# Kernel tuning notes

Measured on AMD Instinct MI355X. Metric: run time of the kernel, lower is better.

The kernel has to match this reference:

```python
import jax, jax.numpy as jnp
import numpy as np

N_NODES = 100000   # number of graph nodes
N_EDGES = 1000000  # number of edges
D_IN = 64          # input feature dim
D_OUT = 64         # output feature dim
N_RELS = 16        # number of relation types


def setup_inputs() -> dict:
    key = jax.random.key(0)
    k1, k2, k3, k4, k5 = jax.random.split(key, 5)
    feat = jax.random.normal(k1, (N_NODES, D_IN), dtype=jnp.float32)
    weight = jax.random.normal(k2, (N_RELS, D_IN, D_OUT), dtype=jnp.float32) * 0.05
    src = jax.random.randint(k3, (N_EDGES,), 0, N_NODES)
    dst = jax.random.randint(k4, (N_EDGES,), 0, N_NODES)
    etypes = jax.random.randint(k5, (N_EDGES,), 0, N_RELS)
    return {"feat": feat, "weight": weight, "src": src, "dst": dst, "etypes": etypes}


def reference(feat, weight, src, dst, etypes):
    # gather source-node features per edge: h = edges.src['h']
    h = feat[src]                                # [E, d_in]
    n_rels = weight.shape[0]
    e, d_out = h.shape[0], weight.shape[2]

    # gather_mm(h, weight, idx_b=etypes): m_e = h_e @ weight[etypes_e]
    # grouped-GEMM realized as R masked dense GEMMs (R is small, fixed);
    # avoids materializing the [E, d_in, d_out] gathered weight tensor.
    def step(m, rw):
        r, w_r = rw
        mask = jnp.where(etypes == r, 1.0, 0.0).astype(h.dtype)  # [E]
        m = m + mask[:, None] * (h @ w_r)                        # [E, d_out]
        return m, None

    m0 = jnp.zeros((e, d_out), dtype=h.dtype)
    m, _ = jax.lax.scan(step, m0, (jnp.arange(n_rels), weight))

    # update_all(..., fn.sum('m', 'h')): scatter-sum messages to dst nodes
    out = jax.ops.segment_sum(m, dst, num_segments=feat.shape[0])  # [N, d_out]
    return out
```

## Files before the change

kernel.cpp:

```cpp
#include <hip/hip_runtime.h>
#include <hip/hip_bf16.h>
#include <stdint.h>

#define NNODES 100000
#define NEDGES 1000000
#define NRELS 16
#define EPB 2048
#define NB ((NEDGES + EPB - 1) / EPB)
#define PADCAP (NEDGES + NRELS * 64)
#define MAXTILES (PADCAP / 64)
#define NDN NNODES
#define BKT 256
#define NBKT ((NDN + BKT - 1) / BKT)

#define FEAT_BLKS 6250
#define W_BLKS 256
#define SETUP_BLKS (FEAT_BLKS + W_BLKS + NB)
#define SCANS_BLKS (1 + (NBKT + 15) / 16)

#define WS_NEED 157070848ull

using short8  = __attribute__((ext_vector_type(8))) short;
using floatx4 = __attribute__((ext_vector_type(4))) float;
using uintx4  = __attribute__((ext_vector_type(4))) unsigned int;

__device__ __forceinline__ unsigned short f2bf(float f) {
    union { float f; uint32_t u; } v; v.f = f;
    uint32_t u = v.u;
    return (unsigned short)((u + 0x7FFFu + ((u >> 16) & 1u)) >> 16);
}
__device__ __forceinline__ float bf2f(uint32_t u16) {
    union { uint32_t u; float f; } v; v.u = u16 << 16;
    return v.f;
}
__device__ __forceinline__ uint32_t pk2(float a, float b) {
    __hip_bfloat162 h = __float22bfloat162_rn(make_float2(a, b));
    union { __hip_bfloat162 h; uint32_t u; } v; v.h = h;
    return v.u;
}

__global__ void k_setup(const float* __restrict__ feat, const float* __restrict__ W,
                        const int* __restrict__ et, const int* __restrict__ dst,
                        unsigned short* __restrict__ featB, unsigned short* __restrict__ Wt,
                        int* __restrict__ hist16, int* __restrict__ hist391) {
    __shared__ int cnt16[16];
    __shared__ int cnt391[NBKT];
    const int b = blockIdx.x;
    if (b < FEAT_BLKS) {
        int i = (b * 256 + threadIdx.x) * 4;
        const float4 f = *(const float4*)(feat + i);
        ushort4 o;
        o.x = f2bf(f.x); o.y = f2bf(f.y); o.z = f2bf(f.z); o.w = f2bf(f.w);
        *(ushort4*)(featB + i) = o;
    } else if (b < FEAT_BLKS + W_BLKS) {
        int t = (b - FEAT_BLKS) * 256 + threadIdx.x;
        int r = t >> 12, n = (t >> 6) & 63, k = t & 63;
        Wt[t] = f2bf(W[(r << 12) + (k << 6) + n]);
    } else {
        const int bb = b - (FEAT_BLKS + W_BLKS);
        if (threadIdx.x < 16) cnt16[threadIdx.x] = 0;
        for (int t = threadIdx.x; t < NBKT; t += 256) cnt391[t] = 0;
        __syncthreads();
        int start = bb * EPB;
        int end = min(NEDGES, start + EPB);
        for (int i = start + threadIdx.x; i < end; i += 256) {
            atomicAdd(&cnt16[et[i]], 1);
            atomicAdd(&cnt391[dst[i] >> 8], 1);
        }
        __syncthreads();
        if (threadIdx.x < 16) hist16[bb * 16 + threadIdx.x] = cnt16[threadIdx.x];
        for (int t = threadIdx.x; t < NBKT; t += 256)
            hist391[bb * NBKT + t] = cnt391[t];
    }
}

__global__ void __launch_bounds__(1024)
k_scans(const int* __restrict__ hist16, int* __restrict__ bbase16,
        int* __restrict__ Pve,
        const int* __restrict__ hist391, int* __restrict__ bbase391,
        int* __restrict__ bstart) {
    int w = threadIdx.x >> 6;
    int lane = threadIdx.x & 63;
    if (blockIdx.x == 0) {
        __shared__ int s_cnt[16];
        __shared__ int s_P[17];
        int carry = 0;
        for (int c = 0; c < NB; c += 64) {
            int idx = c + lane;
            int v = (idx < NB) ? hist16[idx * 16 + w] : 0;
            int x = v;
            #pragma unroll
            for (int off = 1; off < 64; off <<= 1) {
                int y = __shfl_up(x, off);
                if (lane >= off) x += y;
            }
            if (idx < NB) bbase16[idx * 16 + w] = carry + x - v;
            carry += __shfl(x, 63);
        }
        if (lane == 0) s_cnt[w] = carry;
        __syncthreads();
        if (threadIdx.x == 0) {
            int p = 0;
            for (int r = 0; r < 16; ++r) {
                s_P[r] = p;
                Pve[r] = p;
                Pve[17 + r] = p + s_cnt[r];
                p += (s_cnt[r] + 63) & ~63;
            }
            s_P[16] = p;
            Pve[16] = p;
        }
        __syncthreads();
        int pw = s_P[w];
        for (int idx = lane; idx < NB; idx += 64)
            bbase16[idx * 16 + w] += pw;
    } else {
        int b = (blockIdx.x - 1) * 16 + w;
        if (b >= NBKT) return;
        int carry = 0;
        for (int c = 0; c < NB; c += 64) {
            int idx = c + lane;
            int v = (idx < NB) ? hist391[idx * NBKT + b] : 0;
            int x = v;
            #pragma unroll
            for (int off = 1; off < 64; off <<= 1) {
                int y = __shfl_up(x, off);
                if (lane >= off) x += y;
            }
            if (idx < NB) bbase391[idx * NBKT + b] = carry + x - v;
            carry += __shfl(x, 63);
        }
        if (lane == 0) bstart[b] = carry;
    }
}

__global__ void k_bscanB(int* __restrict__ bstart) {
    __shared__ int wtot[8];
    int t = threadIdx.x;
    int v = (t < NBKT) ? bstart[t] : 0;
    int lane = t & 63, w = t >> 6;
    int x = v;
    #pragma unroll
    for (int off = 1; off < 64; off <<= 1) {
        int y = __shfl_up(x, off);
        if (lane >= off) x += y;
    }
    if (lane == 63) wtot[w] = x;
    __syncthreads();
    int woff = 0;
    for (int i = 0; i < w; ++i) woff += wtot[i];
    if (t < NBKT) bstart[t] = woff + x - v;
    if (t == 511) {
        int total = 0;
        for (int i = 0; i < 8; ++i) total += wtot[i];
        bstart[NBKT] = total;
    }
}

__global__ void k_scatter(const int* __restrict__ et, const int* __restrict__ src,
                          const int* __restrict__ dst, const int* __restrict__ bbase16,
                          const int* __restrict__ bbase391, const int* __restrict__ bstart,
                          int* __restrict__ srcS, int* __restrict__ keyE,
                          unsigned short* __restrict__ dnode) {
    __shared__ int base16[16];
    __shared__ int base391[NBKT];
    if (threadIdx.x < 16) base16[threadIdx.x] = bbase16[blockIdx.x * 16 + threadIdx.x];
    for (int t = threadIdx.x; t < NBKT; t += 256)
        base391[t] = bbase391[blockIdx.x * NBKT + t] + bstart[t];
    __syncthreads();
    int start = blockIdx.x * EPB;
    int end = min(NEDGES, start + EPB);
    for (int i = start + threadIdx.x; i < end; i += 256) {
        int r = et[i];
        int pos = atomicAdd(&base16[r], 1);
        srcS[pos] = src[i];
        int d = dst[i];
        int bp = atomicAdd(&base391[d >> 8], 1);
        keyE[bp] = pos;
        dnode[bp] = (unsigned short)(d & 255);
    }
}

__global__ void __launch_bounds__(256)
k_bsort(const unsigned short* __restrict__ dnode, const int* __restrict__ keyE,
        const int* __restrict__ bstart,
        int* __restrict__ keyS, int* __restrict__ dnstart) {
    __shared__ int cnt[256];
    __shared__ int nodebase[256];
    __shared__ int wtot[4];
    const int b = blockIdx.x;
    const int start = bstart[b], end = bstart[b + 1];
    const int t = threadIdx.x;
    cnt[t] = 0;
    __syncthreads();
    for (int e = start + t; e < end; e += 256)
        atomicAdd(&cnt[dnode[e]], 1);
    __syncthreads();
    int v = cnt[t];
    int lane = t & 63, w = t >> 6;
    int x = v;
    #pragma unroll
    for (int off = 1; off < 64; off <<= 1) {
        int y = __shfl_up(x, off);
        if (lane >= off) x += y;
    }
    if (lane == 63) wtot[w] = x;
    __syncthreads();
    int woff = 0;
    for (int i = 0; i < w; ++i) woff += wtot[i];
    nodebase[t] = woff + x - v;
    cnt[t] = 0;
    __syncthreads();
    dnstart[b * 256 + t] = start + nodebase[t];
    if (b == NBKT - 1 && t == 255) dnstart[NBKT * 256] = end;
    for (int e = start + t; e < end; e += 256) {
        int node = dnode[e];
        int rk = atomicAdd(&cnt[node], 1);
        keyS[start + nodebase[node] + rk] = keyE[e];
    }
}

__global__ void __launch_bounds__(256)
k_computeA(const unsigned short* __restrict__ featB,
           const unsigned short* __restrict__ Wt,
           const int* __restrict__ srcS, const int* __restrict__ Pve,
           unsigned short* __restrict__ msgE) {
    __shared__ float lds[4][16 * 68];
    const int w = threadIdx.x >> 6;
    const int t = blockIdx.x * 4 + w;
    const int base = t * 64;
    const int total = Pve[16];
    if (base >= total) return;
    int r = 0;
    while (base >= Pve[r + 1]) ++r;
    const int validEnd = Pve[17 + r];
    const int lane = threadIdx.x & 63;
    const int quad = lane >> 4;
    const int l16 = lane & 15;

    const unsigned short* wr = Wt + (r << 12);
    short8 bfr[4][2];
    #pragma unroll
    for (int tn = 0; tn < 4; ++tn)
        #pragma unroll
        for (int ks = 0; ks < 2; ++ks)
            bfr[tn][ks] = *(const short8*)(wr + ((tn * 16 + l16) << 6) + ks * 32 + quad * 8);

    const int rr = lane >> 2, seg = lane & 3;
    #pragma unroll
    for (int tm = 0; tm < 4; ++tm) {
        int row = base + tm * 16 + l16;
        int s = (row < validEnd) ? srcS[row] : 0;
        const unsigned short* fp = featB + (s << 6) + quad * 8;
        short8 a0 = *(const short8*)(fp);
        short8 a1 = *(const short8*)(fp + 32);
        #pragma unroll
        for (int tn = 0; tn < 4; ++tn) {
            floatx4 c = {0.f, 0.f, 0.f, 0.f};
            c = __builtin_amdgcn_mfma_f32_16x16x32_bf16(a0, bfr[tn][0], c, 0, 0, 0);
            c = __builtin_amdgcn_mfma_f32_16x16x32_bf16(a1, bfr[tn][1], c, 0, 0, 0);
            #pragma unroll
            for (int j = 0; j < 4; ++j)
                lds[w][(quad * 4 + j) * 68 + tn * 16 + l16] = c[j];
        }
        int grow = base + tm * 16 + rr;
        const float* lp = &lds[w][rr * 68 + seg * 16];
        uintx4 o0, o1;
        o0.x = pk2(lp[0],  lp[1]);  o0.y = pk2(lp[2],  lp[3]);
        o0.z = pk2(lp[4],  lp[5]);  o0.w = pk2(lp[6],  lp[7]);
        o1.x = pk2(lp[8],  lp[9]);  o1.y = pk2(lp[10], lp[11]);
        o1.z = pk2(lp[12], lp[13]); o1.w = pk2(lp[14], lp[15]);
        uintx4* op = (uintx4*)(msgE + (size_t)grow * 64 + seg * 16);
        op[0] = o0;
        op[1] = o1;
    }
}

__global__ void __launch_bounds__(256)
k_reduce(const unsigned short* __restrict__ msgE, const int* __restrict__ keyS,
         const int* __restrict__ dnstart, float* __restrict__ out) {
    int n = blockIdx.x * 4 + (threadIdx.x >> 6);
    if (n >= NDN) return;
    int lane = threadIdx.x & 63;
    int start = dnstart[n];
    int end = dnstart[n + 1];
    int c8 = (lane & 7) * 8;
    float a0 = 0.f, a1 = 0.f, a2 = 0.f, a3 = 0.f;
    float a4 = 0.f, a5 = 0.f, a6 = 0.f, a7 = 0.f;
    for (int row = start + (lane >> 3); row < end; row += 8) {
        int rp = keyS[row];
        uintx4 v = *(const uintx4*)(msgE + (size_t)rp * 64 + c8);
        a0 += bf2f(v.x & 0xffffu); a1 += bf2f(v.x >> 16);
        a2 += bf2f(v.y & 0xffffu); a3 += bf2f(v.y >> 16);
        a4 += bf2f(v.z & 0xffffu); a5 += bf2f(v.z >> 16);
        a6 += bf2f(v.w & 0xffffu); a7 += bf2f(v.w >> 16);
    }
    #pragma unroll
    for (int m = 8; m <= 32; m <<= 1) {
        a0 += __shfl_xor(a0, m); a1 += __shfl_xor(a1, m);
        a2 += __shfl_xor(a2, m); a3 += __shfl_xor(a3, m);
        a4 += __shfl_xor(a4, m); a5 += __shfl_xor(a5, m);
        a6 += __shfl_xor(a6, m); a7 += __shfl_xor(a7, m);
    }
    if (lane < 8) {
        float* op = out + (size_t)n * 64 + lane * 8;
        *(float4*)(op)     = make_float4(a0, a1, a2, a3);
        *(float4*)(op + 4) = make_float4(a4, a5, a6, a7);
    }
}

__global__ void __launch_bounds__(256)
k_fb(const float* __restrict__ feat, const float* __restrict__ W,
     const int* __restrict__ src, const int* __restrict__ dst,
     const int* __restrict__ et, float* __restrict__ out) {
    int e = blockIdx.x * 4 + (threadIdx.x >> 6);
    if (e >= NEDGES) return;
    int c = threadIdx.x & 63;
    int s = src[e], d = dst[e], r = et[e];
    const float* fr = feat + (size_t)s * 64;
    const float* wr = W + ((size_t)r << 12);
    float acc = 0.f;
    for (int k = 0; k < 64; ++k) acc += fr[k] * wr[k * 64 + c];
    atomicAdd(out + (size_t)d * 64 + c, acc);
}

extern "C" void kernel_launch(void* const* d_in, const int* in_sizes, int n_in,
                              void* d_out, int out_size, void* d_ws, size_t ws_size,
                              hipStream_t stream) {
    const float* feat = (const float*)d_in[0];
    const float* W    = (const float*)d_in[1];
    const int* src    = (const int*)d_in[2];
    const int* dst    = (const int*)d_in[3];
    const int* et     = (const int*)d_in[4];
    float* out = (float*)d_out;
    char* ws = (char*)d_ws;

    unsigned short* featB = (unsigned short*)(ws);
    unsigned short* Wt    = (unsigned short*)(ws + 12800000);
    int* hist16   = (int*)(ws + 12931072);
    int* bbase16  = (int*)(ws + 12963840);
    int* Pve      = (int*)(ws + 12996608);
    int* hist391  = (int*)(ws + 12996864);
    int* bbase391 = (int*)(ws + 13764864);
    int* bstart   = (int*)(ws + 14532864);
    unsigned short* dnode = (unsigned short*)(ws + 14534912);
    int* dnstart  = (int*)(ws + 16534912);
    int* keyE     = (int*)(ws + 16935680);
    int* keyS     = (int*)(ws + 20935680);
    int* srcS     = (int*)(ws + 24935680);
    unsigned short* msgE = (unsigned short*)(ws + 28939776);

    if (ws_size >= WS_NEED) {
        k_setup<<<SETUP_BLKS, 256, 0, stream>>>(feat, W, et, dst, featB, Wt,
                                                hist16, hist391);
        k_scans<<<SCANS_BLKS, 1024, 0, stream>>>(hist16, bbase16, Pve, hist391,
                                                 bbase391, bstart);
        k_bscanB<<<1, 512, 0, stream>>>(bstart);
        k_scatter<<<NB, 256, 0, stream>>>(et, src, dst, bbase16, bbase391, bstart,
                                          srcS, keyE, dnode);
        k_bsort<<<NBKT, 256, 0, stream>>>(dnode, keyE, bstart, keyS, dnstart);
        k_computeA<<<(MAXTILES + 3) / 4, 256, 0, stream>>>(featB, Wt, srcS, Pve, msgE);
        k_reduce<<<(NDN + 3) / 4, 256, 0, stream>>>(msgE, keyS, dnstart, out);
    } else {
        hipMemsetAsync(d_out, 0, (size_t)out_size * sizeof(float), stream);
        k_fb<<<(NEDGES + 3) / 4, 256, 0, stream>>>(feat, W, src, dst, et, out);
    }
}
```

Baseline: 235.4 us.

## Scatter messages directly into dst-sorted order and read contiguously in reduce

```diff
diff --git a/kernel.cpp b/kernel.cpp
--- a/kernel.cpp
+++ b/kernel.cpp
@@ -18,7 +18,20 @@
 #define SETUP_BLKS (FEAT_BLKS + W_BLKS + NB)
 #define SCANS_BLKS (1 + (NBKT + 15) / 16)
 
-#define WS_NEED 157070848ull
+#define OFF_FEATB    0ull
+#define OFF_WT       12800000ull
+#define OFF_HIST16   12931072ull
+#define OFF_BBASE16  12963840ull
+#define OFF_PVE      12996608ull
+#define OFF_HIST391  12996864ull
+#define OFF_BBASE391 13764864ull
+#define OFF_BSTART   14532864ull
+#define OFF_DNSTART  14534912ull
+#define OFF_KEYP     14935552ull
+#define OFF_INV      18935552ull
+#define OFF_SRCS     22939648ull
+#define OFF_MSGE     26943744ull
+#define WS_NEED 155074816ull
 
 using short8  = __attribute__((ext_vector_type(8))) short;
 using floatx4 = __attribute__((ext_vector_type(4))) float;
@@ -160,8 +173,7 @@
 __global__ void k_scatter(const int* __restrict__ et, const int* __restrict__ src,
                           const int* __restrict__ dst, const int* __restrict__ bbase16,
                           const int* __restrict__ bbase391, const int* __restrict__ bstart,
-                          int* __restrict__ srcS, int* __restrict__ keyE,
-                          unsigned short* __restrict__ dnode) {
+                          int* __restrict__ srcS, int* __restrict__ keyP) {
     __shared__ int base16[16];
     __shared__ int base391[NBKT];
     if (threadIdx.x < 16) base16[threadIdx.x] = bbase16[blockIdx.x * 16 + threadIdx.x];
@@ -176,15 +188,13 @@
         srcS[pos] = src[i];
         int d = dst[i];
         int bp = atomicAdd(&base391[d >> 8], 1);
-        keyE[bp] = pos;
-        dnode[bp] = (unsigned short)(d & 255);
+        keyP[bp] = (pos << 8) | (d & 255);
     }
 }
 
 __global__ void __launch_bounds__(256)
-k_bsort(const unsigned short* __restrict__ dnode, const int* __restrict__ keyE,
-        const int* __restrict__ bstart,
-        int* __restrict__ keyS, int* __restrict__ dnstart) {
+k_bsort(const int* __restrict__ keyP, const int* __restrict__ bstart,
+        int* __restrict__ inv, int* __restrict__ dnstart) {
     __shared__ int cnt[256];
     __shared__ int nodebase[256];
     __shared__ int wtot[4];
@@ -194,7 +204,7 @@
     cnt[t] = 0;
     __syncthreads();
     for (int e = start + t; e < end; e += 256)
-        atomicAdd(&cnt[dnode[e]], 1);
+        atomicAdd(&cnt[keyP[e] & 255], 1);
     __syncthreads();
     int v = cnt[t];
     int lane = t & 63, w = t >> 6;
@@ -214,9 +224,10 @@
     dnstart[b * 256 + t] = start + nodebase[t];
     if (b == NBKT - 1 && t == 255) dnstart[NBKT * 256] = end;
     for (int e = start + t; e < end; e += 256) {
-        int node = dnode[e];
+        int k = keyP[e];
+        int node = k & 255;
         int rk = atomicAdd(&cnt[node], 1);
-        keyS[start + nodebase[node] + rk] = keyE[e];
+        inv[k >> 8] = start + nodebase[node] + rk;
     }
 }
 
@@ -224,6 +235,7 @@
 k_computeA(const unsigned short* __restrict__ featB,
            const unsigned short* __restrict__ Wt,
            const int* __restrict__ srcS, const int* __restrict__ Pve,
+           const int* __restrict__ inv,
            unsigned short* __restrict__ msgE) {
     __shared__ float lds[4][16 * 68];
     const int w = threadIdx.x >> 6;
@@ -237,7 +249,21 @@
     const int lane = threadIdx.x & 63;
     const int quad = lane >> 4;
     const int l16 = lane & 15;
-
+    const int rr = lane >> 2, seg = lane & 3;
+
+    int s[4];
+    #pragma unroll
+    for (int tm = 0; tm < 4; ++tm) {
+        int row = base + tm * 16 + l16;
+        s[tm] = (row < validEnd) ? srcS[row] : 0;
+    }
+    int dpos[4]; bool vld[4];
+    #pragma unroll
+    for (int tm = 0; tm < 4; ++tm) {
+        int g = base + tm * 16 + rr;
+        vld[tm] = (g < validEnd);
+        dpos[tm] = vld[tm] ? inv[g] : 0;
+    }
     const unsigned short* wr = Wt + (r << 12);
     short8 bfr[4][2];
     #pragma unroll
@@ -245,39 +271,40 @@
         #pragma unroll
         for (int ks = 0; ks < 2; ++ks)
             bfr[tn][ks] = *(const short8*)(wr + ((tn * 16 + l16) << 6) + ks * 32 + quad * 8);
-
-    const int rr = lane >> 2, seg = lane & 3;
+    short8 a[4][2];
     #pragma unroll
     for (int tm = 0; tm < 4; ++tm) {
-        int row = base + tm * 16 + l16;
-        int s = (row < validEnd) ? srcS[row] : 0;
-        const unsigned short* fp = featB + (s << 6) + quad * 8;
-        short8 a0 = *(const short8*)(fp);
-        short8 a1 = *(const short8*)(fp + 32);
+        const unsigned short* fp = featB + ((size_t)s[tm] << 6) + quad * 8;
+        a[tm][0] = *(const short8*)(fp);
+        a[tm][1] = *(const short8*)(fp + 32);
+    }
+    #pragma unroll
+    for (int tm = 0; tm < 4; ++tm) {
         #pragma unroll
         for (int tn = 0; tn < 4; ++tn) {
             floatx4 c = {0.f, 0.f, 0.f, 0.f};
-            c = __builtin_amdgcn_mfma_f32_16x16x32_bf16(a0, bfr[tn][0], c, 0, 0, 0);
-            c = __builtin_amdgcn_mfma_f32_16x16x32_bf16(a1, bfr[tn][1], c, 0, 0, 0);
+            c = __builtin_amdgcn_mfma_f32_16x16x32_bf16(a[tm][0], bfr[tn][0], c, 0, 0, 0);
+            c = __builtin_amdgcn_mfma_f32_16x16x32_bf16(a[tm][1], bfr[tn][1], c, 0, 0, 0);
             #pragma unroll
             for (int j = 0; j < 4; ++j)
                 lds[w][(quad * 4 + j) * 68 + tn * 16 + l16] = c[j];
         }
-        int grow = base + tm * 16 + rr;
-        const float* lp = &lds[w][rr * 68 + seg * 16];
-        uintx4 o0, o1;
-        o0.x = pk2(lp[0],  lp[1]);  o0.y = pk2(lp[2],  lp[3]);
-        o0.z = pk2(lp[4],  lp[5]);  o0.w = pk2(lp[6],  lp[7]);
-        o1.x = pk2(lp[8],  lp[9]);  o1.y = pk2(lp[10], lp[11]);
-        o1.z = pk2(lp[12], lp[13]); o1.w = pk2(lp[14], lp[15]);
-        uintx4* op = (uintx4*)(msgE + (size_t)grow * 64 + seg * 16);
-        op[0] = o0;
-        op[1] = o1;
+        if (vld[tm]) {
+            const float* lp = &lds[w][rr * 68 + seg * 16];
+            uintx4 o0, o1;
+            o0.x = pk2(lp[0],  lp[1]);  o0.y = pk2(lp[2],  lp[3]);
+            o0.z = pk2(lp[4],  lp[5]);  o0.w = pk2(lp[6],  lp[7]);
+            o1.x = pk2(lp[8],  lp[9]);  o1.y = pk2(lp[10], lp[11]);
+            o1.z = pk2(lp[12], lp[13]); o1.w = pk2(lp[14], lp[15]);
+            uintx4* op = (uintx4*)(msgE + (size_t)dpos[tm] * 64 + seg * 16);
+            op[0] = o0;
+            op[1] = o1;
+        }
     }
 }
 
 __global__ void __launch_bounds__(256)
-k_reduce(const unsigned short* __restrict__ msgE, const int* __restrict__ keyS,
+k_reduce(const unsigned short* __restrict__ msgE,
          const int* __restrict__ dnstart, float* __restrict__ out) {
     int n = blockIdx.x * 4 + (threadIdx.x >> 6);
     if (n >= NDN) return;
@@ -287,9 +314,21 @@
     int c8 = (lane & 7) * 8;
     float a0 = 0.f, a1 = 0.f, a2 = 0.f, a3 = 0.f;
     float a4 = 0.f, a5 = 0.f, a6 = 0.f, a7 = 0.f;
-    for (int row = start + (lane >> 3); row < end; row += 8) {
-        int rp = keyS[row];
-        uintx4 v = *(const uintx4*)(msgE + (size_t)rp * 64 + c8);
+    int row = start + (lane >> 3);
+    for (; row + 8 < end; row += 16) {
+        uintx4 v0 = *(const uintx4*)(msgE + (size_t)row * 64 + c8);
+        uintx4 v1 = *(const uintx4*)(msgE + (size_t)(row + 8) * 64 + c8);
+        a0 += bf2f(v0.x & 0xffffu); a1 += bf2f(v0.x >> 16);
+        a2 += bf2f(v0.y & 0xffffu); a3 += bf2f(v0.y >> 16);
+        a4 += bf2f(v0.z & 0xffffu); a5 += bf2f(v0.z >> 16);
+        a6 += bf2f(v0.w & 0xffffu); a7 += bf2f(v0.w >> 16);
+        a0 += bf2f(v1.x & 0xffffu); a1 += bf2f(v1.x >> 16);
+        a2 += bf2f(v1.y & 0xffffu); a3 += bf2f(v1.y >> 16);
+        a4 += bf2f(v1.z & 0xffffu); a5 += bf2f(v1.z >> 16);
+        a6 += bf2f(v1.w & 0xffffu); a7 += bf2f(v1.w >> 16);
+    }
+    if (row < end) {
+        uintx4 v = *(const uintx4*)(msgE + (size_t)row * 64 + c8);
         a0 += bf2f(v.x & 0xffffu); a1 += bf2f(v.x >> 16);
         a2 += bf2f(v.y & 0xffffu); a3 += bf2f(v.y >> 16);
         a4 += bf2f(v.z & 0xffffu); a5 += bf2f(v.z >> 16);
@@ -335,20 +374,19 @@
     float* out = (float*)d_out;
     char* ws = (char*)d_ws;
 
-    unsigned short* featB = (unsigned short*)(ws);
-    unsigned short* Wt    = (unsigned short*)(ws + 12800000);
-    int* hist16   = (int*)(ws + 12931072);
-    int* bbase16  = (int*)(ws + 12963840);
-    int* Pve      = (int*)(ws + 12996608);
-    int* hist391  = (int*)(ws + 12996864);
-    int* bbase391 = (int*)(ws + 13764864);
-    int* bstart   = (int*)(ws + 14532864);
-    unsigned short* dnode = (unsigned short*)(ws + 14534912);
-    int* dnstart  = (int*)(ws + 16534912);
-    int* keyE     = (int*)(ws + 16935680);
-    int* keyS     = (int*)(ws + 20935680);
-    int* srcS     = (int*)(ws + 24935680);
-    unsigned short* msgE = (unsigned short*)(ws + 28939776);
+    unsigned short* featB = (unsigned short*)(ws + OFF_FEATB);
+    unsigned short* Wt    = (unsigned short*)(ws + OFF_WT);
+    int* hist16   = (int*)(ws + OFF_HIST16);
+    int* bbase16  = (int*)(ws + OFF_BBASE16);
+    int* Pve      = (int*)(ws + OFF_PVE);
+    int* hist391  = (int*)(ws + OFF_HIST391);
+    int* bbase391 = (int*)(ws + OFF_BBASE391);
+    int* bstart   = (int*)(ws + OFF_BSTART);
+    int* dnstart  = (int*)(ws + OFF_DNSTART);
+    int* keyP     = (int*)(ws + OFF_KEYP);
+    int* inv      = (int*)(ws + OFF_INV);
+    int* srcS     = (int*)(ws + OFF_SRCS);
+    unsigned short* msgE = (unsigned short*)(ws + OFF_MSGE);
 
     if (ws_size >= WS_NEED) {
         k_setup<<<SETUP_BLKS, 256, 0, stream>>>(feat, W, et, dst, featB, Wt,
@@ -357,10 +395,11 @@
                                                  bbase391, bstart);
         k_bscanB<<<1, 512, 0, stream>>>(bstart);
         k_scatter<<<NB, 256, 0, stream>>>(et, src, dst, bbase16, bbase391, bstart,
-                                          srcS, keyE, dnode);
-        k_bsort<<<NBKT, 256, 0, stream>>>(dnode, keyE, bstart, keyS, dnstart);
-        k_computeA<<<(MAXTILES + 3) / 4, 256, 0, stream>>>(featB, Wt, srcS, Pve, msgE);
-        k_reduce<<<(NDN + 3) / 4, 256, 0, stream>>>(msgE, keyS, dnstart, out);
+                                          srcS, keyP);
+        k_bsort<<<NBKT, 256, 0, stream>>>(keyP, bstart, inv, dnstart);
+        k_computeA<<<(MAXTILES + 3) / 4, 256, 0, stream>>>(featB, Wt, srcS, Pve,
+                                                           inv, msgE);
+        k_reduce<<<(NDN + 3) / 4, 256, 0, stream>>>(msgE, dnstart, out);
     } else {
         hipMemsetAsync(d_out, 0, (size_t)out_size * sizeof(float), stream);
         k_fb<<<(NEDGES + 3) / 4, 256, 0, stream>>>(feat, W, src, dst, et, out);
```

After: 226.5 us. -3.8%, faster.

## Bucket edges by (dst block, relation) and fuse GEMM with LDS scatter-reduce

Applied to the files above, without the earlier changes.

```diff
diff --git a/kernel.cpp b/kernel.cpp
--- a/kernel.cpp
+++ b/kernel.cpp
@@ -7,44 +7,40 @@
 #define NRELS 16
 #define EPB 2048
 #define NB ((NEDGES + EPB - 1) / EPB)
-#define PADCAP (NEDGES + NRELS * 64)
-#define MAXTILES (PADCAP / 64)
 #define NDN NNODES
-#define BKT 256
-#define NBKT ((NDN + BKT - 1) / BKT)
+#define NBK ((NNODES + 127) / 128)
+#define NGRP (NBK * NRELS)
 
 #define FEAT_BLKS 6250
 #define W_BLKS 256
 #define SETUP_BLKS (FEAT_BLKS + W_BLKS + NB)
-#define SCANS_BLKS (1 + (NBKT + 15) / 16)
-
-#define WS_NEED 157070848ull
+#define SCAN_BLKS (NGRP / 16)
+#define PER 13
+
+#define OFF_FEATB   0ull
+#define OFF_WT      12800000ull
+#define OFF_HIST    12931072ull
+#define OFF_BBASE   25167808ull
+#define OFF_COLSUM  37404544ull
+#define OFF_GRP     37454720ull
+#define OFF_SRCD    37504896ull
+#define OFF_LDST    41504896ull
+#define WS_NEED 43504896ull
 
 using short8  = __attribute__((ext_vector_type(8))) short;
 using floatx4 = __attribute__((ext_vector_type(4))) float;
-using uintx4  = __attribute__((ext_vector_type(4))) unsigned int;
 
 __device__ __forceinline__ unsigned short f2bf(float f) {
     union { float f; uint32_t u; } v; v.f = f;
     uint32_t u = v.u;
     return (unsigned short)((u + 0x7FFFu + ((u >> 16) & 1u)) >> 16);
 }
-__device__ __forceinline__ float bf2f(uint32_t u16) {
-    union { uint32_t u; float f; } v; v.u = u16 << 16;
-    return v.f;
-}
-__device__ __forceinline__ uint32_t pk2(float a, float b) {
-    __hip_bfloat162 h = __float22bfloat162_rn(make_float2(a, b));
-    union { __hip_bfloat162 h; uint32_t u; } v; v.h = h;
-    return v.u;
-}
 
 __global__ void k_setup(const float* __restrict__ feat, const float* __restrict__ W,
                         const int* __restrict__ et, const int* __restrict__ dst,
                         unsigned short* __restrict__ featB, unsigned short* __restrict__ Wt,
-                        int* __restrict__ hist16, int* __restrict__ hist391) {
-    __shared__ int cnt16[16];
-    __shared__ int cnt391[NBKT];
+                        unsigned short* __restrict__ histU) {
+    __shared__ int cntG[NGRP];
     const int b = blockIdx.x;
     if (b < FEAT_BLKS) {
         int i = (b * 256 + threadIdx.x) * 4;
@@ -58,88 +54,52 @@
         Wt[t] = f2bf(W[(r << 12) + (k << 6) + n]);
     } else {
         const int bb = b - (FEAT_BLKS + W_BLKS);
-        if (threadIdx.x < 16) cnt16[threadIdx.x] = 0;
-        for (int t = threadIdx.x; t < NBKT; t += 256) cnt391[t] = 0;
+        for (int g = threadIdx.x; g < NGRP; g += 256) cntG[g] = 0;
         __syncthreads();
         int start = bb * EPB;
         int end = min(NEDGES, start + EPB);
-        for (int i = start + threadIdx.x; i < end; i += 256) {
-            atomicAdd(&cnt16[et[i]], 1);
-            atomicAdd(&cnt391[dst[i] >> 8], 1);
+        for (int i = start + threadIdx.x; i < end; i += 256)
+            atomicAdd(&cntG[(dst[i] >> 7) * 16 + et[i]], 1);
+        __syncthreads();
+        for (int g = threadIdx.x; g < NGRP; g += 256)
+            histU[(size_t)bb * NGRP + g] = (unsigned short)cntG[g];
+    }
+}
+
+__global__ void __launch_bounds__(1024)
+k_scans(const unsigned short* __restrict__ histU, unsigned short* __restrict__ bbaseU,
+        int* __restrict__ colsum) {
+    int w = threadIdx.x >> 6, lane = threadIdx.x & 63;
+    int col = blockIdx.x * 16 + w;
+    int carry = 0;
+    for (int c = 0; c < NB; c += 64) {
+        int idx = c + lane;
+        int v = (idx < NB) ? (int)histU[(size_t)idx * NGRP + col] : 0;
+        int x = v;
+        #pragma unroll
+        for (int off = 1; off < 64; off <<= 1) {
+            int y = __shfl_up(x, off);
+            if (lane >= off) x += y;
         }
-        __syncthreads();
-        if (threadIdx.x < 16) hist16[bb * 16 + threadIdx.x] = cnt16[threadIdx.x];
-        for (int t = threadIdx.x; t < NBKT; t += 256)
-            hist391[bb * NBKT + t] = cnt391[t];
-    }
+        if (idx < NB) bbaseU[(size_t)idx * NGRP + col] = (unsigned short)(carry + x - v);
+        carry += __shfl(x, 63);
+    }
+    if (lane == 0) colsum[col] = carry;
 }
 
 __global__ void __launch_bounds__(1024)
-k_scans(const int* __restrict__ hist16, int* __restrict__ bbase16,
-        int* __restrict__ Pve,
-        const int* __restrict__ hist391, int* __restrict__ bbase391,
-        int* __restrict__ bstart) {
-    int w = threadIdx.x >> 6;
-    int lane = threadIdx.x & 63;
-    if (blockIdx.x == 0) {
-        __shared__ int s_cnt[16];
-        __shared__ int s_P[17];
-        int carry = 0;
-        for (int c = 0; c < NB; c += 64) {
-            int idx = c + lane;
-            int v = (idx < NB) ? hist16[idx * 16 + w] : 0;
-            int x = v;
-            #pragma unroll
-            for (int off = 1; off < 64; off <<= 1) {
-                int y = __shfl_up(x, off);
-                if (lane >= off) x += y;
-            }
-            if (idx < NB) bbase16[idx * 16 + w] = carry + x - v;
-            carry += __shfl(x, 63);
-        }
-        if (lane == 0) s_cnt[w] = carry;
-        __syncthreads();
-        if (threadIdx.x == 0) {
-            int p = 0;
-            for (int r = 0; r < 16; ++r) {
-                s_P[r] = p;
-                Pve[r] = p;
-                Pve[17 + r] = p + s_cnt[r];
-                p += (s_cnt[r] + 63) & ~63;
-            }
-            s_P[16] = p;
-            Pve[16] = p;
-        }
-        __syncthreads();
-        int pw = s_P[w];
-        for (int idx = lane; idx < NB; idx += 64)
-            bbase16[idx * 16 + w] += pw;
-    } else {
-        int b = (blockIdx.x - 1) * 16 + w;
-        if (b >= NBKT) return;
-        int carry = 0;
-        for (int c = 0; c < NB; c += 64) {
-            int idx = c + lane;
-            int v = (idx < NB) ? hist391[idx * NBKT + b] : 0;
-            int x = v;
-            #pragma unroll
-            for (int off = 1; off < 64; off <<= 1) {
-                int y = __shfl_up(x, off);
-                if (lane >= off) x += y;
-            }
-            if (idx < NB) bbase391[idx * NBKT + b] = carry + x - v;
-            carry += __shfl(x, 63);
-        }
-        if (lane == 0) bstart[b] = carry;
-    }
-}
-
-__global__ void k_bscanB(int* __restrict__ bstart) {
-    __shared__ int wtot[8];
+k_scanB(const int* __restrict__ colsum, int* __restrict__ grpstart) {
+    __shared__ int wtot[16];
     int t = threadIdx.x;
-    int v = (t < NBKT) ? bstart[t] : 0;
+    int v[PER]; int sum = 0;
+    #pragma unroll
+    for (int i = 0; i < PER; ++i) {
+        int idx = t * PER + i;
+        int x = (idx < NGRP) ? colsum[idx] : 0;
+        v[i] = sum; sum += x;
+    }
     int lane = t & 63, w = t >> 6;
-    int x = v;
+    int x = sum;
     #pragma unroll
     for (int off = 1; off < 64; off <<= 1) {
         int y = __shfl_up(x, off);
@@ -149,163 +109,92 @@
     __syncthreads();
     int woff = 0;
     for (int i = 0; i < w; ++i) woff += wtot[i];
-    if (t < NBKT) bstart[t] = woff + x - v;
-    if (t == 511) {
-        int total = 0;
-        for (int i = 0; i < 8; ++i) total += wtot[i];
-        bstart[NBKT] = total;
-    }
+    int excl = woff + x - sum;
+    #pragma unroll
+    for (int i = 0; i < PER; ++i) {
+        int idx = t * PER + i;
+        if (idx < NGRP) grpstart[idx] = excl + v[i];
+    }
+    if (t == 1023) grpstart[NGRP] = excl + sum;
 }
 
 __global__ void k_scatter(const int* __restrict__ et, const int* __restrict__ src,
-                          const int* __restrict__ dst, const int* __restrict__ bbase16,
-                          const int* __restrict__ bbase391, const int* __restrict__ bstart,
-                          int* __restrict__ srcS, int* __restrict__ keyE,
-                          unsigned short* __restrict__ dnode) {
-    __shared__ int base16[16];
-    __shared__ int base391[NBKT];
-    if (threadIdx.x < 16) base16[threadIdx.x] = bbase16[blockIdx.x * 16 + threadIdx.x];
-    for (int t = threadIdx.x; t < NBKT; t += 256)
-        base391[t] = bbase391[blockIdx.x * NBKT + t] + bstart[t];
+                          const int* __restrict__ dst,
+                          const unsigned short* __restrict__ bbaseU,
+                          const int* __restrict__ grpstart,
+                          int* __restrict__ srcD, unsigned short* __restrict__ ldst) {
+    __shared__ int base[NGRP];
+    for (int g = threadIdx.x; g < NGRP; g += 256)
+        base[g] = grpstart[g] + (int)bbaseU[(size_t)blockIdx.x * NGRP + g];
     __syncthreads();
     int start = blockIdx.x * EPB;
     int end = min(NEDGES, start + EPB);
     for (int i = start + threadIdx.x; i < end; i += 256) {
-        int r = et[i];
-        int pos = atomicAdd(&base16[r], 1);
-        srcS[pos] = src[i];
         int d = dst[i];
-        int bp = atomicAdd(&base391[d >> 8], 1);
-        keyE[bp] = pos;
-        dnode[bp] = (unsigned short)(d & 255);
+        int g = (d >> 7) * 16 + et[i];
+        int pos = atomicAdd(&base[g], 1);
+        srcD[pos] = src[i];
+        ldst[pos] = (unsigned short)(d & 127);
     }
 }
 
 __global__ void __launch_bounds__(256)
-k_bsort(const unsigned short* __restrict__ dnode, const int* __restrict__ keyE,
-        const int* __restrict__ bstart,
-        int* __restrict__ keyS, int* __restrict__ dnstart) {
-    __shared__ int cnt[256];
-    __shared__ int nodebase[256];
-    __shared__ int wtot[4];
+k_fused(const unsigned short* __restrict__ featB,
+        const unsigned short* __restrict__ Wt,
+        const int* __restrict__ srcD, const unsigned short* __restrict__ ldst,
+        const int* __restrict__ grpstart, float* __restrict__ out) {
+    __shared__ float acc[128 * 68];
+    __shared__ int gs[17];
     const int b = blockIdx.x;
-    const int start = bstart[b], end = bstart[b + 1];
     const int t = threadIdx.x;
-    cnt[t] = 0;
-    __syncthreads();
-    for (int e = start + t; e < end; e += 256)
-        atomicAdd(&cnt[dnode[e]], 1);
-    __syncthreads();
-    int v = cnt[t];
-    int lane = t & 63, w = t >> 6;
-    int x = v;
-    #pragma unroll
-    for (int off = 1; off < 64; off <<= 1) {
-        int y = __shfl_up(x, off);
-        if (lane >= off) x += y;
-    }
-    if (lane == 63) wtot[w] = x;
-    __syncthreads();
-    int woff = 0;
-    for (int i = 0; i < w; ++i) woff += wtot[i];
-    nodebase[t] = woff + x - v;
-    cnt[t] = 0;
-    __syncthreads();
-    dnstart[b * 256 + t] = start + nodebase[t];
-    if (b == NBKT - 1 && t == 255) dnstart[NBKT * 256] = end;
-    for (int e = start + t; e < end; e += 256) {
-        int node = dnode[e];
-        int rk = atomicAdd(&cnt[node], 1);
-        keyS[start + nodebase[node] + rk] = keyE[e];
-    }
-}
-
-__global__ void __launch_bounds__(256)
-k_computeA(const unsigned short* __restrict__ featB,
-           const unsigned short* __restrict__ Wt,
-           const int* __restrict__ srcS, const int* __restrict__ Pve,
-           unsigned short* __restrict__ msgE) {
-    __shared__ float lds[4][16 * 68];
-    const int w = threadIdx.x >> 6;
-    const int t = blockIdx.x * 4 + w;
-    const int base = t * 64;
-    const int total = Pve[16];
-    if (base >= total) return;
-    int r = 0;
-    while (base >= Pve[r + 1]) ++r;
-    const int validEnd = Pve[17 + r];
-    const int lane = threadIdx.x & 63;
-    const int quad = lane >> 4;
-    const int l16 = lane & 15;
-
-    const unsigned short* wr = Wt + (r << 12);
-    short8 bfr[4][2];
-    #pragma unroll
-    for (int tn = 0; tn < 4; ++tn)
+    const int w = t >> 6, lane = t & 63;
+    const int quad = lane >> 4, l16 = lane & 15;
+    if (t < 17) gs[t] = grpstart[b * 16 + t];
+    for (int i = t; i < 128 * 68; i += 256) acc[i] = 0.f;
+    __syncthreads();
+    #pragma unroll
+    for (int rq = 0; rq < 4; ++rq) {
+        int rel = w * 4 + rq;
+        int rs = gs[rel], re = gs[rel + 1];
+        if (rs >= re) continue;
+        const unsigned short* wr = Wt + (rel << 12);
+        short8 bfr[4][2];
         #pragma unroll
-        for (int ks = 0; ks < 2; ++ks)
-            bfr[tn][ks] = *(const short8*)(wr + ((tn * 16 + l16) << 6) + ks * 32 + quad * 8);
-
-    const int rr = lane >> 2, seg = lane & 3;
-    #pragma unroll
-    for (int tm = 0; tm < 4; ++tm) {
-        int row = base + tm * 16 + l16;
-        int s = (row < validEnd) ? srcS[row] : 0;
-        const unsigned short* fp = featB + (s << 6) + quad * 8;
-        short8 a0 = *(const short8*)(fp);
-        short8 a1 = *(const short8*)(fp + 32);
+        for (int tn = 0; tn < 4; ++tn)
+            #pragma unroll
+            for (int ks = 0; ks < 2; ++ks)
+                bfr[tn][ks] = *(const short8*)(wr + ((tn * 16 + l16) << 6) + ks * 32 + quad * 8);
+        for (int tile = rs; tile < re; tile += 16) {
+            int e = tile + l16;
+            bool vl = e < re;
+            int s  = vl ? srcD[e] : 0;
+            int ld = vl ? (int)ldst[e] : 0;
+            const unsigned short* fp = featB + ((size_t)s << 6) + quad * 8;
+            short8 a0 = *(const short8*)fp;
+            short8 a1 = *(const short8*)(fp + 32);
+            #pragma unroll
+            for (int tn = 0; tn < 4; ++tn) {
+                floatx4 c = {0.f, 0.f, 0.f, 0.f};
+                c = __builtin_amdgcn_mfma_f32_16x16x32_bf16(a0, bfr[tn][0], c, 0, 0, 0);
+                c = __builtin_amdgcn_mfma_f32_16x16x32_bf16(a1, bfr[tn][1], c, 0, 0, 0);
+                #pragma unroll
+                for (int j = 0; j < 4; ++j) {
+                    int ej = quad * 4 + j;
+                    int lj = __shfl(ld, ej);
+                    if (tile + ej < re)
+                        atomicAdd(&acc[lj * 68 + tn * 16 + l16], c[j]);
+                }
+            }
+        }
+    }
+    __syncthreads();
+    int n = b * 128 + (t >> 1);
+    if (n < NDN) {
+        const float* lp = &acc[(t >> 1) * 68 + (t & 1) * 32];
+        float* op = out + (size_t)n * 64 + (t & 1) * 32;
         #pragma unroll
-        for (int tn = 0; tn < 4; ++tn) {
-            floatx4 c = {0.f, 0.f, 0.f, 0.f};
-            c = __builtin_amdgcn_mfma_f32_16x16x32_bf16(a0, bfr[tn][0], c, 0, 0, 0);
-            c = __builtin_amdgcn_mfma_f32_16x16x32_bf16(a1, bfr[tn][1], c, 0, 0, 0);
-            #pragma unroll
-            for (int j = 0; j < 4; ++j)
-                lds[w][(quad * 4 + j) * 68 + tn * 16 + l16] = c[j];
-        }
-        int grow = base + tm * 16 + rr;
-        const float* lp = &lds[w][rr * 68 + seg * 16];
-        uintx4 o0, o1;
-        o0.x = pk2(lp[0],  lp[1]);  o0.y = pk2(lp[2],  lp[3]);
-        o0.z = pk2(lp[4],  lp[5]);  o0.w = pk2(lp[6],  lp[7]);
-        o1.x = pk2(lp[8],  lp[9]);  o1.y = pk2(lp[10], lp[11]);
-        o1.z = pk2(lp[12], lp[13]); o1.w = pk2(lp[14], lp[15]);
-        uintx4* op = (uintx4*)(msgE + (size_t)grow * 64 + seg * 16);
-        op[0] = o0;
-        op[1] = o1;
-    }
-}
-
-__global__ void __launch_bounds__(256)
-k_reduce(const unsigned short* __restrict__ msgE, const int* __restrict__ keyS,
-         const int* __restrict__ dnstart, float* __restrict__ out) {
-    int n = blockIdx.x * 4 + (threadIdx.x >> 6);
-    if (n >= NDN) return;
-    int lane = threadIdx.x & 63;
-    int start = dnstart[n];
-    int end = dnstart[n + 1];
-    int c8 = (lane & 7) * 8;
-    float a0 = 0.f, a1 = 0.f, a2 = 0.f, a3 = 0.f;
-    float a4 = 0.f, a5 = 0.f, a6 = 0.f, a7 = 0.f;
-    for (int row = start + (lane >> 3); row < end; row += 8) {
-        int rp = keyS[row];
-        uintx4 v = *(const uintx4*)(msgE + (size_t)rp * 64 + c8);
-        a0 += bf2f(v.x & 0xffffu); a1 += bf2f(v.x >> 16);
-        a2 += bf2f(v.y & 0xffffu); a3 += bf2f(v.y >> 16);
-        a4 += bf2f(v.z & 0xffffu); a5 += bf2f(v.z >> 16);
-        a6 += bf2f(v.w & 0xffffu); a7 += bf2f(v.w >> 16);
-    }
-    #pragma unroll
-    for (int m = 8; m <= 32; m <<= 1) {
-        a0 += __shfl_xor(a0, m); a1 += __shfl_xor(a1, m);
-        a2 += __shfl_xor(a2, m); a3 += __shfl_xor(a3, m);
-        a4 += __shfl_xor(a4, m); a5 += __shfl_xor(a5, m);
-        a6 += __shfl_xor(a6, m); a7 += __shfl_xor(a7, m);
-    }
-    if (lane < 8) {
-        float* op = out + (size_t)n * 64 + lane * 8;
-        *(float4*)(op)     = make_float4(a0, a1, a2, a3);
-        *(float4*)(op + 4) = make_float4(a4, a5, a6, a7);
+        for (int i = 0; i < 8; ++i)
+            *(float4*)(op + i * 4) = *(const float4*)(lp + i * 4);
     }
 }
 
@@ -335,32 +224,21 @@
     float* out = (float*)d_out;
     char* ws = (char*)d_ws;
 
-    unsigned short* featB = (unsigned short*)(ws);
-    unsigned short* Wt    = (unsigned short*)(ws + 12800000);
-    int* hist16   = (int*)(ws + 12931072);
-    int* bbase16  = (int*)(ws + 12963840);
-    int* Pve      = (int*)(ws + 12996608);
-    int* hist391  = (int*)(ws + 12996864);
-    int* bbase391 = (int*)(ws + 13764864);
-    int* bstart   = (int*)(ws + 14532864);
-    unsigned short* dnode = (unsigned short*)(ws + 14534912);
-    int* dnstart  = (int*)(ws + 16534912);
-    int* keyE     = (int*)(ws + 16935680);
-    int* keyS     = (int*)(ws + 20935680);
-    int* srcS     = (int*)(ws + 24935680);
-    unsigned short* msgE = (unsigned short*)(ws + 28939776);
+    unsigned short* featB  = (unsigned short*)(ws + OFF_FEATB);
+    unsigned short* Wt     = (unsigned short*)(ws + OFF_WT);
+    unsigned short* histU  = (unsigned short*)(ws + OFF_HIST);
+    unsigned short* bbaseU = (unsigned short*)(ws + OFF_BBASE);
+    int* colsum   = (int*)(ws + OFF_COLSUM);
+    int* grpstart = (int*)(ws + OFF_GRP);
+    int* srcD     = (int*)(ws + OFF_SRCD);
+    unsigned short* ldst = (unsigned short*)(ws + OFF_LDST);
 
     if (ws_size >= WS_NEED) {
-        k_setup<<<SETUP_BLKS, 256, 0, stream>>>(feat, W, et, dst, featB, Wt,
-                                                hist16, hist391);
-        k_scans<<<SCANS_BLKS, 1024, 0, stream>>>(hist16, bbase16, Pve, hist391,
-                                                 bbase391, bstart);
-        k_bscanB<<<1, 512, 0, stream>>>(bstart);
-        k_scatter<<<NB, 256, 0, stream>>>(et, src, dst, bbase16, bbase391, bstart,
-                                          srcS, keyE, dnode);
-        k_bsort<<<NBKT, 256, 0, stream>>>(dnode, keyE, bstart, keyS, dnstart);
-        k_computeA<<<(MAXTILES + 3) / 4, 256, 0, stream>>>(featB, Wt, srcS, Pve, msgE);
-        k_reduce<<<(NDN + 3) / 4, 256, 0, stream>>>(msgE, keyS, dnstart, out);
+        k_setup<<<SETUP_BLKS, 256, 0, stream>>>(feat, W, et, dst, featB, Wt, histU);
+        k_scans<<<SCAN_BLKS, 1024, 0, stream>>>(histU, bbaseU, colsum);
+        k_scanB<<<1, 1024, 0, stream>>>(colsum, grpstart);
+        k_scatter<<<NB, 256, 0, stream>>>(et, src, dst, bbaseU, grpstart, srcD, ldst);
+        k_fused<<<NBK, 256, 0, stream>>>(featB, Wt, srcD, ldst, grpstart, out);
     } else {
         hipMemsetAsync(d_out, 0, (size_t)out_size * sizeof(float), stream);
         k_fb<<<(NEDGES + 3) / 4, 256, 0, stream>>>(feat, W, src, dst, et, out);
```

Result: slower. 634.2 us (+169.4%).
